# Kernel tuning notes

Measured on AMD Instinct MI355X. Metric: run time of the kernel, lower is better.

Reference implementation:

```python
import jax, jax.numpy as jnp
import numpy as np

B, S, D, H, E, K = 2, 2048, 512, 2048, 16, 2
LN_EPS = 1e-5


def setup_inputs() -> dict:
    key = jax.random.key(0)
    ks = jax.random.split(key, 9)
    s_in = 1.0 / np.sqrt(D)
    s_hid = 1.0 / np.sqrt(H)
    return {
        "x": jax.random.normal(ks[0], (B, S, D), dtype=jnp.float32),
        "Wg": jax.random.normal(ks[1], (D, E), dtype=jnp.float32) * s_in,
        "bg": jax.random.normal(ks[2], (E,), dtype=jnp.float32) * 0.01,
        "W1": jax.random.normal(ks[3], (E, D, H), dtype=jnp.float32) * s_in,
        "b1": jax.random.normal(ks[4], (E, H), dtype=jnp.float32) * 0.01,
        "W2": jax.random.normal(ks[5], (E, H, D), dtype=jnp.float32) * s_hid,
        "b2": jax.random.normal(ks[6], (E, D), dtype=jnp.float32) * 0.01,
        "gamma": jnp.ones((D,), dtype=jnp.float32),
        "beta": jnp.zeros((D,), dtype=jnp.float32),
    }


def reference(x, Wg, bg, W1, b1, W2, b2, gamma, beta):
    # --- top-k gating (GatingFuncTopK) ---
    logits = jnp.einsum("bsd,de->bse", x, Wg) + bg            # [B,S,E]
    probs = jax.nn.softmax(logits, axis=-1)
    topk_vals, topk_idx = jax.lax.top_k(probs, K)             # [B,S,K]
    # scatter top-k probs back into a sparse [B,S,E] routing matrix
    sparse = (jax.nn.one_hot(topk_idx, E, dtype=probs.dtype)
              * topk_vals[..., None]).sum(axis=-2)            # [B,S,E]

    # --- dense all-expert FFN (stack over experts, as in the torch code) ---
    h = jax.nn.relu(jnp.einsum("bsd,edh->ebsh", x, W1)
                    + b1[:, None, None, :])                   # [E,B,S,H]
    ex = jnp.einsum("ebsh,ehd->ebsd", h, W2) + b2[:, None, None, :]  # [E,B,S,D]

    # --- weighted combine + residual + layernorm ---
    out = jnp.einsum("bse,ebsd->bsd", sparse, ex) + x
    mu = out.mean(axis=-1, keepdims=True)
    var = ((out - mu) ** 2).mean(axis=-1, keepdims=True)
    out = (out - mu) * jax.lax.rsqrt(var + LN_EPS) * gamma + beta
    return out
```

## Files before the change

### kernel.cpp

```cpp
#include <hip/hip_runtime.h>
#include <math.h>

#define NTOK 4096
#define DDIM 512
#define HDIM 2048
#define NEXP 16


#define WS_COUNTS    0u
#define WS_OFFSETS   1024u
#define WS_NTILES    1280u
#define WS_TM        1536u
#define WS_EPOS      4096u
#define WS_TOK       36864u
#define WS_WL        299008u
#define WS_XA        1048576u
#define WS_W1T       11534336u
#define WS_W2T       45088768u
#define WS_HB        78643200u
#define WS_YB        WS_W1T

typedef __attribute__((ext_vector_type(8))) short short8;
typedef __attribute__((ext_vector_type(4))) float floatx4;
typedef unsigned short ushort_t;

__device__ __forceinline__ ushort_t f2bf(float f) {
    unsigned u = __float_as_uint(f);
    u += 0x7fffu + ((u >> 16) & 1u);
    return (ushort_t)(u >> 16);
}
__device__ __forceinline__ float bf2f(ushort_t u) {
    return __uint_as_float((unsigned)u << 16);
}

__device__ __forceinline__ void gld16(const void* g, void* l) {
    __builtin_amdgcn_global_load_lds(
        (const __attribute__((address_space(1))) unsigned*)g,
        (__attribute__((address_space(3))) unsigned*)l, 16, 0, 0);
}

#define WAIT4_BAR() asm volatile("s_waitcnt vmcnt(4)\n\ts_barrier" ::: "memory")
#define WAIT0_BAR() asm volatile("s_waitcnt vmcnt(0)\n\ts_barrier" ::: "memory")

__device__ __forceinline__ void wtrans_tile(
    const float* __restrict__ src, ushort_t* __restrict__ dst,
    int C, int NT, int CK, int e, int ks, int nw, unsigned* lb, int tid)
{
    const int q = tid >> 4;
    const int c0 = (tid & 15) << 2;
    const float* sp = src + (size_t)e * (DDIM * HDIM)
                    + (size_t)(ks * 32 + 2 * q) * C + nw * 256;
    float4 va[4], vb[4];
    #pragma unroll
    for (int p = 0; p < 4; ++p) {
        va[p] = *(const float4*)(sp + c0 + p * 64);
        vb[p] = *(const float4*)(sp + C + c0 + p * 64);
    }
    #pragma unroll
    for (int p = 0; p < 4; ++p) {
        const int n = c0 + p * 64;
        lb[(n + 0) * 17 + q] = (unsigned)f2bf(va[p].x) | ((unsigned)f2bf(vb[p].x) << 16);
        lb[(n + 1) * 17 + q] = (unsigned)f2bf(va[p].y) | ((unsigned)f2bf(vb[p].y) << 16);
        lb[(n + 2) * 17 + q] = (unsigned)f2bf(va[p].z) | ((unsigned)f2bf(vb[p].z) << 16);
        lb[(n + 3) * 17 + q] = (unsigned)f2bf(va[p].w) | ((unsigned)f2bf(vb[p].w) << 16);
    }
    __syncthreads();
    const int nt = tid >> 4, nl = tid & 15;
    const int ntg = nw * 16 + nt;
    ushort_t* rbase = dst + ((size_t)e * NT + ntg) * ((size_t)CK * 128) + nl * 8;
    const unsigned* rp = lb + (nt * 16 + nl) * 17;
    #pragma unroll
    for (int kc = 0; kc < 4; ++kc) {
        const unsigned o0 = rp[kc * 4 + 0], o1 = rp[kc * 4 + 1];
        const unsigned o2 = rp[kc * 4 + 2], o3 = rp[kc * 4 + 3];
        *(uint4*)(rbase + (size_t)(ks * 4 + kc) * 128) = make_uint4(o0, o1, o2, o3);
    }
}

__global__ __launch_bounds__(256) void fusedA_kernel(
    const float* __restrict__ x, const float* __restrict__ Wg,
    const float* __restrict__ bg, int* __restrict__ counts,
    int* __restrict__ tok_list, float* __restrict__ w_list,
    int* __restrict__ epos, const float* __restrict__ W1,
    ushort_t* __restrict__ W1t)
{
    __shared__ __align__(16) float smem[4416];
    __shared__ int lcnt[16], lbase[16];
    const int tid = threadIdx.x;
    int bid = blockIdx.x;

    if (bid >= 512) {
        bid -= 512;
        const int e = bid >> 7, r = bid & 127;
        const int nw = r & 7, ks = r >> 3;
        wtrans_tile(W1, W1t, HDIM, 128, 64, e, ks, nw, (unsigned*)smem, tid);
        return;
    }

    float (*xs)[520] = (float(*)[520])smem;
    float (*lsm)[16][2] = (float(*)[16][2])(smem + 4160);
    const int t0 = bid * 8;
    const float* xg = x + (size_t)t0 * DDIM;
    #pragma unroll
    for (int p = 0; p < 4; ++p) {
        const int idx = p * 1024 + tid * 4;
        *(float4*)&xs[idx >> 9][idx & 511] = *(const float4*)(xg + idx);
    }
    if (tid < 16) lcnt[tid] = 0;
    __syncthreads();
    const int tl = tid >> 5, e = (tid >> 1) & 15, h = tid & 1;
    float a0 = 0.f, a1 = 0.f, a2 = 0.f, a3 = 0.f;
    #pragma unroll 8
    for (int it = 0; it < 64; ++it) {
        const int d = h * 256 + it * 4;
        const float4 xv = *(const float4*)&xs[tl][d];
        a0 = fmaf(xv.x, Wg[(d + 0) * 16 + e], a0);
        a1 = fmaf(xv.y, Wg[(d + 1) * 16 + e], a1);
        a2 = fmaf(xv.z, Wg[(d + 2) * 16 + e], a2);
        a3 = fmaf(xv.w, Wg[(d + 3) * 16 + e], a3);
    }
    lsm[tl][e][h] = (a0 + a1) + (a2 + a3);
    __syncthreads();

    int i0 = 0, i1 = -1, r0 = 0, r1 = 0;
    float w0 = 0.f, w1 = 0.f;
    const bool tokth = ((tid & 31) == 0);
    if (tokth) {
        float l[16];
        #pragma unroll
        for (int j = 0; j < NEXP; ++j) l[j] = lsm[tl][j][0] + lsm[tl][j][1] + bg[j];
        float m = -1e30f;
        #pragma unroll
        for (int j = 0; j < NEXP; ++j) m = fmaxf(m, l[j]);
        float s = 0.f;
        #pragma unroll
        for (int j = 0; j < NEXP; ++j) s += __expf(l[j] - m);
        float v0 = -1e30f;
        #pragma unroll
        for (int j = 0; j < NEXP; ++j)
            if (l[j] > v0) { v0 = l[j]; i0 = j; }
        float v1 = -1e30f;
        #pragma unroll
        for (int j = 0; j < NEXP; ++j)
            if (j != i0 && l[j] > v1) { v1 = l[j]; i1 = j; }
        w0 = __expf(v0 - m) / s;
        w1 = __expf(v1 - m) / s;
        r0 = atomicAdd(&lcnt[i0], 1);
        r1 = atomicAdd(&lcnt[i1], 1);
    }
    __syncthreads();
    if (tid < 16 && lcnt[tid] > 0)
        lbase[tid] = atomicAdd(&counts[tid * 16], lcnt[tid]);
    __syncthreads();
    if (tokth) {
        const int t = t0 + tl;
        const int p0 = lbase[i0] + r0;
        tok_list[i0 * NTOK + p0] = t;
        w_list[i0 * NTOK + p0] = w0;
        epos[t * 2 + 0] = (i0 << 16) | p0;
        const int p1 = lbase[i1] + r1;
        tok_list[i1 * NTOK + p1] = t;
        w_list[i1 * NTOK + p1] = w1;
        epos[t * 2 + 1] = (i1 << 16) | p1;
    }
}

__global__ void scan_kernel(const int* __restrict__ counts, int* __restrict__ offsets,
                            int* __restrict__ tm, int* __restrict__ ntiles)
{
    const int lane = threadIdx.x;
    int c = (lane < NEXP) ? counts[lane * 16] : 0;
    int t = (c + 127) >> 7;
    int ic = c, it = t;
    #pragma unroll
    for (int off = 1; off < 16; off <<= 1) {
        const int pc = __shfl_up(ic, off, 64);
        const int pt = __shfl_up(it, off, 64);
        if (lane >= off) { ic += pc; it += pt; }
    }
    if (lane < NEXP) {
        offsets[lane] = ic - c;
        if (lane == NEXP - 1) { offsets[NEXP] = ic; ntiles[0] = it; }
        const int tb = it - t;
        for (int i = 0; i < t; ++i) tm[tb + i] = (lane << 16) | i;
    }
}

__global__ __launch_bounds__(256) void gather_xa(
    const float* __restrict__ x, const int* __restrict__ tok_list,
    const int* __restrict__ counts, const int* __restrict__ tm,
    const int* __restrict__ ntiles, ushort_t* __restrict__ xa)
{
    const int b = blockIdx.x;
    if (b >= ntiles[0]) return;
    const int info = tm[b];
    const int e = info >> 16, m0 = (info & 0xffff) << 7;
    const int Me = counts[e * 16];
    const int row = threadIdx.x >> 1;
    const int half = threadIdx.x & 1;
    const int kbase = blockIdx.y * 128 + half * 64;
    const int tok = tok_list[e * NTOK + min(m0 + row, Me - 1)];
    const float* src = x + (size_t)tok * DDIM + kbase;
    ushort_t* dstb = xa + (size_t)b * 65536 + (size_t)(row >> 4) * 8192 + (row & 15) * 8;
    #pragma unroll
    for (int q = 0; q < 16; ++q) {
        const int k = kbase + q * 4;
        const float4 v = *(const float4*)(src + q * 4);
        ushort4 o = make_ushort4(f2bf(v.x), f2bf(v.y), f2bf(v.z), f2bf(v.w));
        *(ushort4*)(dstb + (size_t)(k >> 3) * 128 + (k & 7)) = o;
    }
}

__global__ __launch_bounds__(256) void fusedC_kernel(
    const ushort_t* __restrict__ xa, const ushort_t* __restrict__ W1t,
    const float* __restrict__ b1, const int* __restrict__ tm,
    const int* __restrict__ ntiles, ushort_t* __restrict__ hb,
    const float* __restrict__ W2, ushort_t* __restrict__ W2t)
{
    __shared__ __align__(16) ushort_t lds[24576];
    const int tid = threadIdx.x;
    const int bid = blockIdx.x;

    if (bid >= 1280) {
        const int wb = bid - 1280;
        const int e = wb >> 7, r = wb & 127;
        const int nw = r & 1, ks = r >> 1;
        wtrans_tile(W2, W2t, DDIM, 32, 256, e, ks, nw, (unsigned*)lds, tid);
        return;
    }

    const int swz = (bid & 7) * 160 + (bid >> 3);
    const int t = swz >> 4;
    if (t >= ntiles[0]) return;
    const int e = tm[t] >> 16;
    const int n0 = (swz & 15) << 7;
    const int lane = tid & 63, w = tid >> 6;
    const int fm = lane & 15, fq = lane >> 4;
    const int wr = (w >> 1) << 6, wc = (w & 1) << 6;

    const ushort_t* gA = xa + (size_t)t * 65536 + lane * 8;
    const ushort_t* gB = W1t + ((size_t)e * 128 + (n0 >> 4)) * 8192 + lane * 8;
    const int s0 = w, s1 = w + 4;

    #define G1_STAGE(d, kc) do {                                            \
        ushort_t* lb_ = &lds[(d) * 8192];                                   \
        gld16(gA + (size_t)s0 * 8192 + (kc) * 512, lb_ + s0 * 512);         \
        gld16(gA + (size_t)s1 * 8192 + (kc) * 512, lb_ + s1 * 512);         \
        gld16(gB + (size_t)s0 * 8192 + (kc) * 512, lb_ + 4096 + s0 * 512);  \
        gld16(gB + (size_t)s1 * 8192 + (kc) * 512, lb_ + 4096 + s1 * 512);  \
    } while (0)

    #define G1_COMPUTE(cur) do {                                            \
        const ushort_t* la = &lds[(cur) * 8192 + ((w >> 1) * 4) * 512 + lane * 8]; \
        const ushort_t* lbB = &lds[(cur) * 8192 + 4096 + ((w & 1) * 4) * 512 + lane * 8]; \
        short8 af[4], bf[4];                                                \
        _Pragma("unroll")                                                   \
        for (int i = 0; i < 4; ++i) af[i] = *(const short8*)(la + i * 512); \
        _Pragma("unroll")                                                   \
        for (int j = 0; j < 4; ++j) bf[j] = *(const short8*)(lbB + j * 512);\
        _Pragma("unroll")                                                   \
        for (int i = 0; i < 4; ++i)                                         \
            _Pragma("unroll")                                               \
            for (int j = 0; j < 4; ++j)                                     \
                acc[i][j] = __builtin_amdgcn_mfma_f32_16x16x32_bf16(        \
                    af[i], bf[j], acc[i][j], 0, 0, 0);                      \
    } while (0)

    G1_STAGE(0, 0);
    G1_STAGE(1, 1);
    floatx4 acc[4][4] = {};
    int cur = 0;
    #pragma unroll 1
    for (int kc = 0; kc < 14; ++kc) {
        WAIT4_BAR();
        const int nb = (kc + 2) % 3;
        G1_STAGE(nb, kc + 2);
        G1_COMPUTE(cur);
        cur = (cur == 2) ? 0 : cur + 1;
    }
    WAIT4_BAR();
    G1_COMPUTE(cur);
    cur = (cur == 2) ? 0 : cur + 1;
    WAIT0_BAR();
    G1_COMPUTE(cur);
    __syncthreads();
    #undef G1_STAGE
    #undef G1_COMPUTE

    ushort_t* ls = lds;
    #pragma unroll
    for (int j = 0; j < 4; ++j) {
        const float bias = b1[(size_t)e * HDIM + n0 + wc + j * 16 + fm];
        #pragma unroll
        for (int i = 0; i < 4; ++i)
            #pragma unroll
            for (int r = 0; r < 4; ++r) {
                const int row = wr + i * 16 + fq * 4 + r;
                ls[row * 128 + wc + j * 16 + fm] =
                    f2bf(fmaxf(acc[i][j][r] + bias, 0.f));
            }
    }
    __syncthreads();
    ushort_t* hbase = hb + (size_t)t * 262144 + (size_t)(n0 >> 3) * 128;
    #pragma unroll
    for (int p = 0; p < 8; ++p) {
        const int unit = tid + p * 256;
        const int row = unit >> 4, c16 = unit & 15;
        *(short8*)(hbase + (size_t)(row >> 4) * 32768 + (size_t)c16 * 128
                   + (row & 15) * 8) = *(const short8*)&ls[row * 128 + c16 * 8];
    }
}

__global__ __launch_bounds__(256) void gemm2_mfma(
    const ushort_t* __restrict__ hb, const ushort_t* __restrict__ W2t,
    const float* __restrict__ b2, const float* __restrict__ w_list,
    const int* __restrict__ counts, const int* __restrict__ offsets,
    const int* __restrict__ tm, const int* __restrict__ ntiles,
    ushort_t* __restrict__ yb)
{
    const int bid = blockIdx.x;
    const int swz = (bid & 7) * 160 + (bid >> 3);
    const int n0i = swz & 3;
    const int q = swz >> 2;
    const int kz = q / 80;
    const int t = q - kz * 80;
    if (t >= ntiles[0]) return;
    const int info = tm[t];
    const int e = info >> 16, m0 = (info & 0xffff) << 7;
    const int Me = counts[e * 16], aoff = offsets[e];
    const int n0 = n0i << 7;
    const int tid = threadIdx.x, lane = tid & 63, w = tid >> 6;
    const int fm = lane & 15, fq = lane >> 4;
    const int wr = (w >> 1) << 6, wc = (w & 1) << 6;

    __shared__ __align__(16) ushort_t lds[24576];

    const ushort_t* gA = hb + (size_t)t * 262144 + (size_t)kz * 8192 + lane * 8;
    const ushort_t* gB = W2t + ((size_t)e * 32 + (n0 >> 4)) * 32768
                       + (size_t)kz * 8192 + lane * 8;
    const int s0 = w, s1 = w + 4;

    #define G2_STAGE(d, kc) do {                                            \
        ushort_t* lb_ = &lds[(d) * 8192];                                   \
        gld16(gA + (size_t)s0 * 32768 + (kc) * 512, lb_ + s0 * 512);        \
        gld16(gA + (size_t)s1 * 32768 + (kc) * 512, lb_ + s1 * 512);        \
        gld16(gB + (size_t)s0 * 32768 + (kc) * 512, lb_ + 4096 + s0 * 512); \
        gld16(gB + (size_t)s1 * 32768 + (kc) * 512, lb_ + 4096 + s1 * 512); \
    } while (0)

    #define G2_COMPUTE(cur) do {                                            \
        const ushort_t* la = &lds[(cur) * 8192 + ((w >> 1) * 4) * 512 + lane * 8]; \
        const ushort_t* lbB = &lds[(cur) * 8192 + 4096 + ((w & 1) * 4) * 512 + lane * 8]; \
        short8 af[4], bf[4];                                                \
        _Pragma("unroll")                                                   \
        for (int i = 0; i < 4; ++i) af[i] = *(const short8*)(la + i * 512); \
        _Pragma("unroll")                                                   \
        for (int j = 0; j < 4; ++j) bf[j] = *(const short8*)(lbB + j * 512);\
        _Pragma("unroll")                                                   \
        for (int i = 0; i < 4; ++i)                                         \
            _Pragma("unroll")                                               \
            for (int j = 0; j < 4; ++j)                                     \
                acc[i][j] = __builtin_amdgcn_mfma_f32_16x16x32_bf16(        \
                    af[i], bf[j], acc[i][j], 0, 0, 0);                      \
    } while (0)

    G2_STAGE(0, 0);
    G2_STAGE(1, 1);
    floatx4 acc[4][4] = {};
    int cur = 0;
    #pragma unroll 1
    for (int kc = 0; kc < 14; ++kc) {
        WAIT4_BAR();
        const int nb = (kc + 2) % 3;
        G2_STAGE(nb, kc + 2);
        G2_COMPUTE(cur);
        cur = (cur == 2) ? 0 : cur + 1;
    }
    WAIT4_BAR();
    G2_COMPUTE(cur);
    cur = (cur == 2) ? 0 : cur + 1;
    WAIT0_BAR();
    G2_COMPUTE(cur);
    __syncthreads();
    #undef G2_STAGE
    #undef G2_COMPUTE

    ushort_t* ls = lds;
    #pragma unroll
    for (int j = 0; j < 4; ++j) {
        const float bias = (kz == 0) ? b2[(size_t)e * DDIM + n0 + wc + j * 16 + fm] : 0.f;
        #pragma unroll
        for (int i = 0; i < 4; ++i)
            #pragma unroll
            for (int r = 0; r < 4; ++r) {
                const int row = wr + i * 16 + fq * 4 + r;
                const float gw = w_list[e * NTOK + min(m0 + row, Me - 1)];
                ls[row * 128 + wc + j * 16 + fm] = f2bf(gw * (acc[i][j][r] + bias));
            }
    }
    __syncthreads();
    ushort_t* ybase = yb + (size_t)kz * (8192 * 512) + n0;
    #pragma unroll
    for (int p = 0; p < 8; ++p) {
        const int unit = tid + p * 256;
        const int row = unit >> 4, c16 = unit & 15;
        if (m0 + row < Me)
            *(short8*)(ybase + (size_t)(aoff + m0 + row) * 512 + c16 * 8)
                = *(const short8*)&ls[row * 128 + c16 * 8];
    }
}

__global__ __launch_bounds__(256) void ln_kernel(
    const float* __restrict__ x, const ushort_t* __restrict__ yb,
    const int* __restrict__ epos, const int* __restrict__ offsets,
    const float* __restrict__ gamma, const float* __restrict__ beta,
    float* __restrict__ out)
{
    const int t = blockIdx.x * 4 + (threadIdx.x >> 6);
    const int lane = threadIdx.x & 63;
    const int d0 = lane * 8;

    const int p0 = epos[2 * t + 0];
    const int p1 = epos[2 * t + 1];
    const size_t r0 = (size_t)(offsets[p0 >> 16] + (p0 & 0xFFFF));
    const size_t r1 = (size_t)(offsets[p1 >> 16] + (p1 & 0xFFFF));

    short8 ys[8];
    #pragma unroll
    for (int kz = 0; kz < 4; ++kz) {
        ys[kz * 2 + 0] = *(const short8*)(yb + (size_t)kz * (8192 * 512) + r0 * 512 + d0);
        ys[kz * 2 + 1] = *(const short8*)(yb + (size_t)kz * (8192 * 512) + r1 * 512 + d0);
    }
    float xv[8];
    *(float4*)&xv[0] = *(const float4*)(x + (size_t)t * DDIM + d0);
    *(float4*)&xv[4] = *(const float4*)(x + (size_t)t * DDIM + d0 + 4);

    float v[8];
    float s = 0.f;
    #pragma unroll
    for (int i = 0; i < 8; ++i) {
        float a = xv[i];
        #pragma unroll
        for (int q = 0; q < 8; ++q) a += bf2f((ushort_t)ys[q][i]);
        v[i] = a;
        s += a;
    }
    #pragma unroll
    for (int o = 32; o > 0; o >>= 1) s += __shfl_xor(s, o, 64);
    const float mu = s * (1.f / DDIM);
    float q = 0.f;
    #pragma unroll
    for (int i = 0; i < 8; ++i) { const float d_ = v[i] - mu; q = fmaf(d_, d_, q); }
    #pragma unroll
    for (int o = 32; o > 0; o >>= 1) q += __shfl_xor(q, o, 64);
    const float rstd = rsqrtf(q * (1.f / DDIM) + 1e-5f);

    float g[8], bt[8], o8[8];
    *(float4*)&g[0] = *(const float4*)(gamma + d0);
    *(float4*)&g[4] = *(const float4*)(gamma + d0 + 4);
    *(float4*)&bt[0] = *(const float4*)(beta + d0);
    *(float4*)&bt[4] = *(const float4*)(beta + d0 + 4);
    #pragma unroll
    for (int i = 0; i < 8; ++i) o8[i] = (v[i] - mu) * rstd * g[i] + bt[i];
    *(float4*)(out + (size_t)t * DDIM + d0) = *(float4*)&o8[0];
    *(float4*)(out + (size_t)t * DDIM + d0 + 4) = *(float4*)&o8[4];
}

extern "C" void kernel_launch(void* const* d_in, const int* in_sizes, int n_in,
                              void* d_out, int out_size, void* d_ws, size_t ws_size,
                              hipStream_t stream) {
    const float* x     = (const float*)d_in[0];
    const float* Wg    = (const float*)d_in[1];
    const float* bg    = (const float*)d_in[2];
    const float* W1    = (const float*)d_in[3];
    const float* b1    = (const float*)d_in[4];
    const float* W2    = (const float*)d_in[5];
    const float* b2    = (const float*)d_in[6];
    const float* gamma = (const float*)d_in[7];
    const float* beta  = (const float*)d_in[8];
    float* out = (float*)d_out;

    char* ws = (char*)d_ws;
    int*      counts   = (int*)(ws + WS_COUNTS);
    int*      offsets  = (int*)(ws + WS_OFFSETS);
    int*      ntiles   = (int*)(ws + WS_NTILES);
    int*      tm       = (int*)(ws + WS_TM);
    int*      epos     = (int*)(ws + WS_EPOS);
    int*      tok_list = (int*)(ws + WS_TOK);
    float*    w_list   = (float*)(ws + WS_WL);
    ushort_t* xa       = (ushort_t*)(ws + WS_XA);
    ushort_t* W1t      = (ushort_t*)(ws + WS_W1T);
    ushort_t* W2t      = (ushort_t*)(ws + WS_W2T);
    ushort_t* hb       = (ushort_t*)(ws + WS_HB);
    ushort_t* yb       = (ushort_t*)(ws + WS_YB);

    hipMemsetAsync(counts, 0, 1024, stream);
    fusedA_kernel<<<2560, 256, 0, stream>>>(x, Wg, bg, counts, tok_list, w_list,
                                            epos, W1, W1t);
    scan_kernel<<<1, 64, 0, stream>>>(counts, offsets, tm, ntiles);
    gather_xa<<<dim3(80, 4), 256, 0, stream>>>(x, tok_list, counts, tm, ntiles, xa);
    fusedC_kernel<<<3328, 256, 0, stream>>>(xa, W1t, b1, tm, ntiles, hb, W2, W2t);
    gemm2_mfma<<<1280, 256, 0, stream>>>(
        hb, W2t, b2, w_list, counts, offsets, tm, ntiles, yb);
    ln_kernel<<<NTOK / 4, 256, 0, stream>>>(x, yb, epos, offsets, gamma, beta, out);
}
```

Baseline: 263.2 us.

## Fuse fp32 weight bf16 conversion into grouped GEMM B-tile loads

Removes the separate passes that transposed and converted W1 and W2 to bf16 into workspace, which were folded into the gating and GEMM1 launches. Each GEMM now reads fp32 weight rows directly into registers, packs them to bf16 and writes them transposed into a double-buffered padded LDS tile, while activations still stream through a triple-buffered async-to-LDS pipeline. This saves the extra write and read of the bf16 weight copies. In exchange, each GEMM tile reads fp32 weights, twice the bytes, and does the conversion per tile, so weights shared by many token tiles are converted repeatedly. Launch bounds requesting 3 blocks per CU were also added.

Measured after the change: 279.1 us. +6.0%, slower.

```diff
diff --git a/kernel.cpp b/kernel.cpp
--- a/kernel.cpp
+++ b/kernel.cpp
@@ -15,10 +15,8 @@
 #define WS_TOK       36864u
 #define WS_WL        299008u
 #define WS_XA        1048576u
-#define WS_W1T       11534336u
-#define WS_W2T       45088768u
+#define WS_YB        11534336u
 #define WS_HB        78643200u
-#define WS_YB        WS_W1T
 
 typedef __attribute__((ext_vector_type(8))) short short8;
 typedef __attribute__((ext_vector_type(4))) float floatx4;
@@ -32,6 +30,9 @@
 __device__ __forceinline__ float bf2f(ushort_t u) {
     return __uint_as_float((unsigned)u << 16);
 }
+__device__ __forceinline__ unsigned pk2(float a, float b) {
+    return (unsigned)f2bf(a) | ((unsigned)f2bf(b) << 16);
+}
 
 __device__ __forceinline__ void gld16(const void* g, void* l) {
     __builtin_amdgcn_global_load_lds(
@@ -39,63 +40,22 @@
         (__attribute__((address_space(3))) unsigned*)l, 16, 0, 0);
 }
 
-#define WAIT4_BAR() asm volatile("s_waitcnt vmcnt(4)\n\ts_barrier" ::: "memory")
-#define WAIT0_BAR() asm volatile("s_waitcnt vmcnt(0)\n\ts_barrier" ::: "memory")
-
-__device__ __forceinline__ void wtrans_tile(
-    const float* __restrict__ src, ushort_t* __restrict__ dst,
-    int C, int NT, int CK, int e, int ks, int nw, unsigned* lb, int tid)
-{
-    const int q = tid >> 4;
-    const int c0 = (tid & 15) << 2;
-    const float* sp = src + (size_t)e * (DDIM * HDIM)
-                    + (size_t)(ks * 32 + 2 * q) * C + nw * 256;
-    float4 va[4], vb[4];
-    #pragma unroll
-    for (int p = 0; p < 4; ++p) {
-        va[p] = *(const float4*)(sp + c0 + p * 64);
-        vb[p] = *(const float4*)(sp + C + c0 + p * 64);
-    }
-    #pragma unroll
-    for (int p = 0; p < 4; ++p) {
-        const int n = c0 + p * 64;
-        lb[(n + 0) * 17 + q] = (unsigned)f2bf(va[p].x) | ((unsigned)f2bf(vb[p].x) << 16);
-        lb[(n + 1) * 17 + q] = (unsigned)f2bf(va[p].y) | ((unsigned)f2bf(vb[p].y) << 16);
-        lb[(n + 2) * 17 + q] = (unsigned)f2bf(va[p].z) | ((unsigned)f2bf(vb[p].z) << 16);
-        lb[(n + 3) * 17 + q] = (unsigned)f2bf(va[p].w) | ((unsigned)f2bf(vb[p].w) << 16);
-    }
-    __syncthreads();
-    const int nt = tid >> 4, nl = tid & 15;
-    const int ntg = nw * 16 + nt;
-    ushort_t* rbase = dst + ((size_t)e * NT + ntg) * ((size_t)CK * 128) + nl * 8;
-    const unsigned* rp = lb + (nt * 16 + nl) * 17;
-    #pragma unroll
-    for (int kc = 0; kc < 4; ++kc) {
-        const unsigned o0 = rp[kc * 4 + 0], o1 = rp[kc * 4 + 1];
-        const unsigned o2 = rp[kc * 4 + 2], o3 = rp[kc * 4 + 3];
-        *(uint4*)(rbase + (size_t)(ks * 4 + kc) * 128) = make_uint4(o0, o1, o2, o3);
-    }
-}
-
-__global__ __launch_bounds__(256) void fusedA_kernel(
+#define WAIT2()  asm volatile("s_waitcnt vmcnt(2)" ::: "memory")
+#define WAIT0()  asm volatile("s_waitcnt vmcnt(0)" ::: "memory")
+#define LGKM_BAR() asm volatile("s_waitcnt lgkmcnt(0)\n\ts_barrier" ::: "memory")
+
+union U8 { unsigned u[4]; short8 s; };
+
+__global__ __launch_bounds__(256) void gating_kernel(
     const float* __restrict__ x, const float* __restrict__ Wg,
     const float* __restrict__ bg, int* __restrict__ counts,
     int* __restrict__ tok_list, float* __restrict__ w_list,
-    int* __restrict__ epos, const float* __restrict__ W1,
-    ushort_t* __restrict__ W1t)
+    int* __restrict__ epos)
 {
     __shared__ __align__(16) float smem[4416];
     __shared__ int lcnt[16], lbase[16];
     const int tid = threadIdx.x;
-    int bid = blockIdx.x;
-
-    if (bid >= 512) {
-        bid -= 512;
-        const int e = bid >> 7, r = bid & 127;
-        const int nw = r & 7, ks = r >> 3;
-        wtrans_tile(W1, W1t, HDIM, 128, 64, e, ks, nw, (unsigned*)smem, tid);
-        return;
-    }
+    const int bid = blockIdx.x;
 
     float (*xs)[520] = (float(*)[520])smem;
     float (*lsm)[16][2] = (float(*)[16][2])(smem + 4160);
@@ -211,81 +171,106 @@
     }
 }
 
-__global__ __launch_bounds__(256) void fusedC_kernel(
-    const ushort_t* __restrict__ xa, const ushort_t* __restrict__ W1t,
+__global__ __launch_bounds__(256, 3) void gemm1_mfma(
+    const ushort_t* __restrict__ xa, const float* __restrict__ W1,
     const float* __restrict__ b1, const int* __restrict__ tm,
-    const int* __restrict__ ntiles, ushort_t* __restrict__ hb,
-    const float* __restrict__ W2, ushort_t* __restrict__ W2t)
+    const int* __restrict__ ntiles, ushort_t* __restrict__ hb)
 {
-    __shared__ __align__(16) ushort_t lds[24576];
-    const int tid = threadIdx.x;
     const int bid = blockIdx.x;
-
-    if (bid >= 1280) {
-        const int wb = bid - 1280;
-        const int e = wb >> 7, r = wb & 127;
-        const int nw = r & 1, ks = r >> 1;
-        wtrans_tile(W2, W2t, DDIM, 32, 256, e, ks, nw, (unsigned*)lds, tid);
-        return;
-    }
-
     const int swz = (bid & 7) * 160 + (bid >> 3);
     const int t = swz >> 4;
     if (t >= ntiles[0]) return;
     const int e = tm[t] >> 16;
     const int n0 = (swz & 15) << 7;
-    const int lane = tid & 63, w = tid >> 6;
+    const int tid = threadIdx.x, lane = tid & 63, w = tid >> 6;
     const int fm = lane & 15, fq = lane >> 4;
     const int wr = (w >> 1) << 6, wc = (w & 1) << 6;
 
+    __shared__ __align__(16) ushort_t lds[20992];
+    ushort_t* Al = lds;
+    unsigned* Bb = (unsigned*)(lds + 12288);
+
     const ushort_t* gA = xa + (size_t)t * 65536 + lane * 8;
-    const ushort_t* gB = W1t + ((size_t)e * 128 + (n0 >> 4)) * 8192 + lane * 8;
     const int s0 = w, s1 = w + 4;
-
-    #define G1_STAGE(d, kc) do {                                            \
-        ushort_t* lb_ = &lds[(d) * 8192];                                   \
-        gld16(gA + (size_t)s0 * 8192 + (kc) * 512, lb_ + s0 * 512);         \
-        gld16(gA + (size_t)s1 * 8192 + (kc) * 512, lb_ + s1 * 512);         \
-        gld16(gB + (size_t)s0 * 8192 + (kc) * 512, lb_ + 4096 + s0 * 512);  \
-        gld16(gB + (size_t)s1 * 8192 + (kc) * 512, lb_ + 4096 + s1 * 512);  \
-    } while (0)
-
-    #define G1_COMPUTE(cur) do {                                            \
-        const ushort_t* la = &lds[(cur) * 8192 + ((w >> 1) * 4) * 512 + lane * 8]; \
-        const ushort_t* lbB = &lds[(cur) * 8192 + 4096 + ((w & 1) * 4) * 512 + lane * 8]; \
-        short8 af[4], bf[4];                                                \
+    const float* gB = W1 + (size_t)e * (DDIM * HDIM) + n0;
+    const int qa = tid >> 5, ca4 = (tid & 31) << 2;
+
+    float4 bvv[4];
+
+    #define AGLD(k) do {                                                    \
+        ushort_t* ab_ = Al + ((k) % 3) * 4096;                              \
+        gld16(gA + (size_t)s0 * 8192 + (k) * 512, ab_ + s0 * 512);          \
+        gld16(gA + (size_t)s1 * 8192 + (k) * 512, ab_ + s1 * 512);          \
+    } while (0)
+
+    #define BLOAD(k) do {                                                   \
+        const float* r0_ = gB + (size_t)((k) * 32 + 2 * qa) * HDIM + ca4;   \
+        const float* r1_ = gB + (size_t)((k) * 32 + 2 * qa + 16) * HDIM + ca4; \
+        bvv[0] = *(const float4*)r0_;                                       \
+        bvv[1] = *(const float4*)(r0_ + HDIM);                              \
+        bvv[2] = *(const float4*)r1_;                                       \
+        bvv[3] = *(const float4*)(r1_ + HDIM);                              \
+    } while (0)
+
+    #define BWRITE(k) do {                                                  \
+        unsigned* BL_ = Bb + ((k) & 1) * 2176;                              \
+        BL_[(ca4 + 0) * 17 + qa] = pk2(bvv[0].x, bvv[1].x);                 \
+        BL_[(ca4 + 1) * 17 + qa] = pk2(bvv[0].y, bvv[1].y);                 \
+        BL_[(ca4 + 2) * 17 + qa] = pk2(bvv[0].z, bvv[1].z);                 \
+        BL_[(ca4 + 3) * 17 + qa] = pk2(bvv[0].w, bvv[1].w);                 \
+        BL_[(ca4 + 0) * 17 + qa + 8] = pk2(bvv[2].x, bvv[3].x);             \
+        BL_[(ca4 + 1) * 17 + qa + 8] = pk2(bvv[2].y, bvv[3].y);             \
+        BL_[(ca4 + 2) * 17 + qa + 8] = pk2(bvv[2].z, bvv[3].z);             \
+        BL_[(ca4 + 3) * 17 + qa + 8] = pk2(bvv[2].w, bvv[3].w);             \
+    } while (0)
+
+    #define COMPUTE(k) do {                                                 \
+        const ushort_t* la_ = Al + ((k) % 3) * 4096 + ((w >> 1) * 4) * 512 + lane * 8; \
+        const unsigned* bb_ = Bb + ((k) & 1) * 2176                         \
+                            + ((w & 1) * 64 + (lane & 15)) * 17 + (lane >> 4) * 4; \
+        short8 af[4];                                                       \
         _Pragma("unroll")                                                   \
-        for (int i = 0; i < 4; ++i) af[i] = *(const short8*)(la + i * 512); \
+        for (int i = 0; i < 4; ++i) af[i] = *(const short8*)(la_ + i * 512);\
         _Pragma("unroll")                                                   \
-        for (int j = 0; j < 4; ++j) bf[j] = *(const short8*)(lbB + j * 512);\
-        _Pragma("unroll")                                                   \
-        for (int i = 0; i < 4; ++i)                                         \
+        for (int j = 0; j < 4; ++j) {                                       \
+            U8 tb_;                                                         \
+            tb_.u[0] = bb_[j * 272 + 0]; tb_.u[1] = bb_[j * 272 + 1];       \
+            tb_.u[2] = bb_[j * 272 + 2]; tb_.u[3] = bb_[j * 272 + 3];       \
+            const short8 bf_ = tb_.s;                                       \
             _Pragma("unroll")                                               \
-            for (int j = 0; j < 4; ++j)                                     \
+            for (int i = 0; i < 4; ++i)                                     \
                 acc[i][j] = __builtin_amdgcn_mfma_f32_16x16x32_bf16(        \
-                    af[i], bf[j], acc[i][j], 0, 0, 0);                      \
-    } while (0)
-
-    G1_STAGE(0, 0);
-    G1_STAGE(1, 1);
+                    af[i], bf_, acc[i][j], 0, 0, 0);                        \
+        }                                                                   \
+    } while (0)
+
+    #define STEP(k, WM) do {                                                \
+        WM();                              \
+        BWRITE(k);                                                          \
+        LGKM_BAR();                                                         \
+        if ((k) < 15) BLOAD((k) + 1);                                       \
+        if ((k) < 14) AGLD((k) + 2);                                        \
+        COMPUTE(k);                                                         \
+    } while (0)
+
+    BLOAD(0);
+    AGLD(0);
+    AGLD(1);
+
     floatx4 acc[4][4] = {};
-    int cur = 0;
     #pragma unroll 1
-    for (int kc = 0; kc < 14; ++kc) {
-        WAIT4_BAR();
-        const int nb = (kc + 2) % 3;
-        G1_STAGE(nb, kc + 2);
-        G1_COMPUTE(cur);
-        cur = (cur == 2) ? 0 : cur + 1;
-    }
-    WAIT4_BAR();
-    G1_COMPUTE(cur);
-    cur = (cur == 2) ? 0 : cur + 1;
-    WAIT0_BAR();
-    G1_COMPUTE(cur);
-    __syncthreads();
-    #undef G1_STAGE
-    #undef G1_COMPUTE
+    for (int kc = 0; kc < 14; kc += 2) {
+        STEP(kc, WAIT2);
+        STEP(kc + 1, WAIT2);
+    }
+    STEP(14, WAIT2);
+    STEP(15, WAIT0);
+    __syncthreads();
+    #undef AGLD
+    #undef BLOAD
+    #undef BWRITE
+    #undef COMPUTE
+    #undef STEP
 
     ushort_t* ls = lds;
     #pragma unroll
@@ -311,8 +296,8 @@
     }
 }
 
-__global__ __launch_bounds__(256) void gemm2_mfma(
-    const ushort_t* __restrict__ hb, const ushort_t* __restrict__ W2t,
+__global__ __launch_bounds__(256, 3) void gemm2_mfma(
+    const ushort_t* __restrict__ hb, const float* __restrict__ W2,
     const float* __restrict__ b2, const float* __restrict__ w_list,
     const int* __restrict__ counts, const int* __restrict__ offsets,
     const int* __restrict__ tm, const int* __restrict__ ntiles,
@@ -321,9 +306,9 @@
     const int bid = blockIdx.x;
     const int swz = (bid & 7) * 160 + (bid >> 3);
     const int n0i = swz & 3;
-    const int q = swz >> 2;
-    const int kz = q / 80;
-    const int t = q - kz * 80;
+    const int q_ = swz >> 2;
+    const int kz = q_ / 80;
+    const int t = q_ - kz * 80;
     if (t >= ntiles[0]) return;
     const int info = tm[t];
     const int e = info >> 16, m0 = (info & 0xffff) << 7;
@@ -333,57 +318,91 @@
     const int fm = lane & 15, fq = lane >> 4;
     const int wr = (w >> 1) << 6, wc = (w & 1) << 6;
 
-    __shared__ __align__(16) ushort_t lds[24576];
+    __shared__ __align__(16) ushort_t lds[20992];
+    ushort_t* Al = lds;
+    unsigned* Bb = (unsigned*)(lds + 12288);
 
     const ushort_t* gA = hb + (size_t)t * 262144 + (size_t)kz * 8192 + lane * 8;
-    const ushort_t* gB = W2t + ((size_t)e * 32 + (n0 >> 4)) * 32768
-                       + (size_t)kz * 8192 + lane * 8;
     const int s0 = w, s1 = w + 4;
-
-    #define G2_STAGE(d, kc) do {                                            \
-        ushort_t* lb_ = &lds[(d) * 8192];                                   \
-        gld16(gA + (size_t)s0 * 32768 + (kc) * 512, lb_ + s0 * 512);        \
-        gld16(gA + (size_t)s1 * 32768 + (kc) * 512, lb_ + s1 * 512);        \
-        gld16(gB + (size_t)s0 * 32768 + (kc) * 512, lb_ + 4096 + s0 * 512); \
-        gld16(gB + (size_t)s1 * 32768 + (kc) * 512, lb_ + 4096 + s1 * 512); \
-    } while (0)
-
-    #define G2_COMPUTE(cur) do {                                            \
-        const ushort_t* la = &lds[(cur) * 8192 + ((w >> 1) * 4) * 512 + lane * 8]; \
-        const ushort_t* lbB = &lds[(cur) * 8192 + 4096 + ((w & 1) * 4) * 512 + lane * 8]; \
-        short8 af[4], bf[4];                                                \
+    const float* gB = W2 + (size_t)e * (DDIM * HDIM) + (size_t)kz * 512 * DDIM + n0;
+    const int qa = tid >> 5, ca4 = (tid & 31) << 2;
+
+    float4 bvv[4];
+
+    #define AGLD(k) do {                                                    \
+        ushort_t* ab_ = Al + ((k) % 3) * 4096;                              \
+        gld16(gA + (size_t)s0 * 32768 + (k) * 512, ab_ + s0 * 512);         \
+        gld16(gA + (size_t)s1 * 32768 + (k) * 512, ab_ + s1 * 512);         \
+    } while (0)
+
+    #define BLOAD(k) do {                                                   \
+        const float* r0_ = gB + (size_t)((k) * 32 + 2 * qa) * DDIM + ca4;   \
+        const float* r1_ = gB + (size_t)((k) * 32 + 2 * qa + 16) * DDIM + ca4; \
+        bvv[0] = *(const float4*)r0_;                                       \
+        bvv[1] = *(const float4*)(r0_ + DDIM);                              \
+        bvv[2] = *(const float4*)r1_;                                       \
+        bvv[3] = *(const float4*)(r1_ + DDIM);                              \
+    } while (0)
+
+    #define BWRITE(k) do {                                                  \
+        unsigned* BL_ = Bb + ((k) & 1) * 2176;                              \
+        BL_[(ca4 + 0) * 17 + qa] = pk2(bvv[0].x, bvv[1].x);                 \
+        BL_[(ca4 + 1) * 17 + qa] = pk2(bvv[0].y, bvv[1].y);                 \
+        BL_[(ca4 + 2) * 17 + qa] = pk2(bvv[0].z, bvv[1].z);                 \
+        BL_[(ca4 + 3) * 17 + qa] = pk2(bvv[0].w, bvv[1].w);                 \
+        BL_[(ca4 + 0) * 17 + qa + 8] = pk2(bvv[2].x, bvv[3].x);             \
+        BL_[(ca4 + 1) * 17 + qa + 8] = pk2(bvv[2].y, bvv[3].y);             \
+        BL_[(ca4 + 2) * 17 + qa + 8] = pk2(bvv[2].z, bvv[3].z);             \
+        BL_[(ca4 + 3) * 17 + qa + 8] = pk2(bvv[2].w, bvv[3].w);             \
+    } while (0)
+
+    #define COMPUTE(k) do {                                                 \
+        const ushort_t* la_ = Al + ((k) % 3) * 4096 + ((w >> 1) * 4) * 512 + lane * 8; \
+        const unsigned* bb_ = Bb + ((k) & 1) * 2176                         \
+                            + ((w & 1) * 64 + (lane & 15)) * 17 + (lane >> 4) * 4; \
+        short8 af[4];                                                       \
         _Pragma("unroll")                                                   \
-        for (int i = 0; i < 4; ++i) af[i] = *(const short8*)(la + i * 512); \
+        for (int i = 0; i < 4; ++i) af[i] = *(const short8*)(la_ + i * 512);\
         _Pragma("unroll")                                                   \
-        for (int j = 0; j < 4; ++j) bf[j] = *(const short8*)(lbB + j * 512);\
-        _Pragma("unroll")                                                   \
-        for (int i = 0; i < 4; ++i)                                         \
+        for (int j = 0; j < 4; ++j) {                                       \
+            U8 tb_;                                                         \
+            tb_.u[0] = bb_[j * 272 + 0]; tb_.u[1] = bb_[j * 272 + 1];       \
+            tb_.u[2] = bb_[j * 272 + 2]; tb_.u[3] = bb_[j * 272 + 3];       \
+            const short8 bf_ = tb_.s;                                       \
             _Pragma("unroll")                                               \
-            for (int j = 0; j < 4; ++j)                                     \
+            for (int i = 0; i < 4; ++i)                                     \
                 acc[i][j] = __builtin_amdgcn_mfma_f32_16x16x32_bf16(        \
-                    af[i], bf[j], acc[i][j], 0, 0, 0);                      \
-    } while (0)
-
-    G2_STAGE(0, 0);
-    G2_STAGE(1, 1);
+                    af[i], bf_, acc[i][j], 0, 0, 0);                        \
+        }                                                                   \
+    } while (0)
+
+    #define STEP(k, WM) do {                                                \
+        WM();                                                               \
+        BWRITE(k);                                                          \
+        LGKM_BAR();                                                         \
+        if ((k) < 15) BLOAD((k) + 1);                                       \
+        if ((k) < 14) AGLD((k) + 2);                                        \
+        COMPUTE(k);                                                         \
+    } while (0)
+
+    BLOAD(0);
+    AGLD(0);
+    AGLD(1);
+
     floatx4 acc[4][4] = {};
-    int cur = 0;
     #pragma unroll 1
-    for (int kc = 0; kc < 14; ++kc) {
-        WAIT4_BAR();
-        const int nb = (kc + 2) % 3;
-        G2_STAGE(nb, kc + 2);
-        G2_COMPUTE(cur);
-        cur = (cur == 2) ? 0 : cur + 1;
-    }
-    WAIT4_BAR();
-    G2_COMPUTE(cur);
-    cur = (cur == 2) ? 0 : cur + 1;
-    WAIT0_BAR();
-    G2_COMPUTE(cur);
-    __syncthreads();
-    #undef G2_STAGE
-    #undef G2_COMPUTE
+    for (int kc = 0; kc < 14; kc += 2) {
+        STEP(kc, WAIT2);
+        STEP(kc + 1, WAIT2);
+    }
+    STEP(14, WAIT2);
+    STEP(15, WAIT0);
+    __syncthreads();
+    #undef AGLD
+    #undef BLOAD
+    #undef BWRITE
+    #undef COMPUTE
+    #undef STEP
 
     ushort_t* ls = lds;
     #pragma unroll
@@ -489,18 +508,15 @@
     int*      tok_list = (int*)(ws + WS_TOK);
     float*    w_list   = (float*)(ws + WS_WL);
     ushort_t* xa       = (ushort_t*)(ws + WS_XA);
-    ushort_t* W1t      = (ushort_t*)(ws + WS_W1T);
-    ushort_t* W2t      = (ushort_t*)(ws + WS_W2T);
+    ushort_t* yb       = (ushort_t*)(ws + WS_YB);
     ushort_t* hb       = (ushort_t*)(ws + WS_HB);
-    ushort_t* yb       = (ushort_t*)(ws + WS_YB);
 
     hipMemsetAsync(counts, 0, 1024, stream);
-    fusedA_kernel<<<2560, 256, 0, stream>>>(x, Wg, bg, counts, tok_list, w_list,
-                                            epos, W1, W1t);
+    gating_kernel<<<512, 256, 0, stream>>>(x, Wg, bg, counts, tok_list, w_list, epos);
     scan_kernel<<<1, 64, 0, stream>>>(counts, offsets, tm, ntiles);
     gather_xa<<<dim3(80, 4), 256, 0, stream>>>(x, tok_list, counts, tm, ntiles, xa);
-    fusedC_kernel<<<3328, 256, 0, stream>>>(xa, W1t, b1, tm, ntiles, hb, W2, W2t);
-    gemm2_mfma<<<1280, 256, 0, stream>>>(
-        hb, W2t, b2, w_list, counts, offsets, tm, ntiles, yb);
+    gemm1_mfma<<<1280, 256, 0, stream>>>(xa, W1, b1, tm, ntiles, hb);
+    gemm2_mfma<<<1280, 256, 0, stream>>>(hb, W2, b2, w_list, counts, offsets,
+                                         tm, ntiles, yb);
     ln_kernel<<<NTOK / 4, 256, 0, stream>>>(x, yb, epos, offsets, gamma, beta, out);
 }
```

## Fuse token gather into GEMM1 and move W2 transpose into first kernel

Applied to the files above, without the earlier changes.

Removes the separate gather_xa kernel. GEMM1 now loads routed token rows of x directly from global memory, converts them to bf16 in registers and writes them into double-buffered LDS, while W1t tiles are still streamed asynchronously into a triple buffer. The W2 transpose work moves from the GEMM1 launch into the gating/W1-transpose kernel, so GEMM1 runs only GEMM tiles. Launch bounds are added for occupancy. The aim is to avoid the xa round trip through global memory and one kernel launch. The cost is register-based A loads that may stall the pipeline, plus a longer first kernel.

After: 299.8 us. 1.14x slower.

```diff
diff --git a/kernel.cpp b/kernel.cpp
--- a/kernel.cpp
+++ b/kernel.cpp
@@ -14,7 +14,6 @@
 #define WS_EPOS      4096u
 #define WS_TOK       36864u
 #define WS_WL        299008u
-#define WS_XA        1048576u
 #define WS_W1T       11534336u
 #define WS_W2T       45088768u
 #define WS_HB        78643200u
@@ -32,6 +31,9 @@
 __device__ __forceinline__ float bf2f(ushort_t u) {
     return __uint_as_float((unsigned)u << 16);
 }
+__device__ __forceinline__ unsigned pk2(float a, float b) {
+    return (unsigned)f2bf(a) | ((unsigned)f2bf(b) << 16);
+}
 
 __device__ __forceinline__ void gld16(const void* g, void* l) {
     __builtin_amdgcn_global_load_lds(
@@ -39,8 +41,10 @@
         (__attribute__((address_space(3))) unsigned*)l, 16, 0, 0);
 }
 
+#define WAIT6_BAR() asm volatile("s_waitcnt vmcnt(6)\n\ts_barrier" ::: "memory")
 #define WAIT4_BAR() asm volatile("s_waitcnt vmcnt(4)\n\ts_barrier" ::: "memory")
 #define WAIT0_BAR() asm volatile("s_waitcnt vmcnt(0)\n\ts_barrier" ::: "memory")
+#define LGKM_BAR()  asm volatile("s_waitcnt lgkmcnt(0)\n\ts_barrier" ::: "memory")
 
 __device__ __forceinline__ void wtrans_tile(
     const float* __restrict__ src, ushort_t* __restrict__ dst,
@@ -59,10 +63,10 @@
     #pragma unroll
     for (int p = 0; p < 4; ++p) {
         const int n = c0 + p * 64;
-        lb[(n + 0) * 17 + q] = (unsigned)f2bf(va[p].x) | ((unsigned)f2bf(vb[p].x) << 16);
-        lb[(n + 1) * 17 + q] = (unsigned)f2bf(va[p].y) | ((unsigned)f2bf(vb[p].y) << 16);
-        lb[(n + 2) * 17 + q] = (unsigned)f2bf(va[p].z) | ((unsigned)f2bf(vb[p].z) << 16);
-        lb[(n + 3) * 17 + q] = (unsigned)f2bf(va[p].w) | ((unsigned)f2bf(vb[p].w) << 16);
+        lb[(n + 0) * 17 + q] = pk2(va[p].x, vb[p].x);
+        lb[(n + 1) * 17 + q] = pk2(va[p].y, vb[p].y);
+        lb[(n + 2) * 17 + q] = pk2(va[p].z, vb[p].z);
+        lb[(n + 3) * 17 + q] = pk2(va[p].w, vb[p].w);
     }
     __syncthreads();
     const int nt = tid >> 4, nl = tid & 15;
@@ -82,13 +86,21 @@
     const float* __restrict__ bg, int* __restrict__ counts,
     int* __restrict__ tok_list, float* __restrict__ w_list,
     int* __restrict__ epos, const float* __restrict__ W1,
-    ushort_t* __restrict__ W1t)
+    ushort_t* __restrict__ W1t, const float* __restrict__ W2,
+    ushort_t* __restrict__ W2t)
 {
     __shared__ __align__(16) float smem[4416];
     __shared__ int lcnt[16], lbase[16];
     const int tid = threadIdx.x;
     int bid = blockIdx.x;
 
+    if (bid >= 2560) {
+        const int wb = bid - 2560;
+        const int e = wb >> 7, r = wb & 127;
+        const int nw = r & 1, ks = r >> 1;
+        wtrans_tile(W2, W2t, DDIM, 32, 256, e, ks, nw, (unsigned*)smem, tid);
+        return;
+    }
     if (bid >= 512) {
         bid -= 512;
         const int e = bid >> 7, r = bid & 127;
@@ -186,78 +198,70 @@
     }
 }
 
-__global__ __launch_bounds__(256) void gather_xa(
+__global__ __launch_bounds__(256, 4) void gemm1_mfma(
     const float* __restrict__ x, const int* __restrict__ tok_list,
+    const ushort_t* __restrict__ W1t, const float* __restrict__ b1,
     const int* __restrict__ counts, const int* __restrict__ tm,
-    const int* __restrict__ ntiles, ushort_t* __restrict__ xa)
+    const int* __restrict__ ntiles, ushort_t* __restrict__ hb)
 {
-    const int b = blockIdx.x;
-    if (b >= ntiles[0]) return;
-    const int info = tm[b];
-    const int e = info >> 16, m0 = (info & 0xffff) << 7;
-    const int Me = counts[e * 16];
-    const int row = threadIdx.x >> 1;
-    const int half = threadIdx.x & 1;
-    const int kbase = blockIdx.y * 128 + half * 64;
-    const int tok = tok_list[e * NTOK + min(m0 + row, Me - 1)];
-    const float* src = x + (size_t)tok * DDIM + kbase;
-    ushort_t* dstb = xa + (size_t)b * 65536 + (size_t)(row >> 4) * 8192 + (row & 15) * 8;
-    #pragma unroll
-    for (int q = 0; q < 16; ++q) {
-        const int k = kbase + q * 4;
-        const float4 v = *(const float4*)(src + q * 4);
-        ushort4 o = make_ushort4(f2bf(v.x), f2bf(v.y), f2bf(v.z), f2bf(v.w));
-        *(ushort4*)(dstb + (size_t)(k >> 3) * 128 + (k & 7)) = o;
-    }
-}
-
-__global__ __launch_bounds__(256) void fusedC_kernel(
-    const ushort_t* __restrict__ xa, const ushort_t* __restrict__ W1t,
-    const float* __restrict__ b1, const int* __restrict__ tm,
-    const int* __restrict__ ntiles, ushort_t* __restrict__ hb,
-    const float* __restrict__ W2, ushort_t* __restrict__ W2t)
-{
-    __shared__ __align__(16) ushort_t lds[24576];
-    const int tid = threadIdx.x;
     const int bid = blockIdx.x;
-
-    if (bid >= 1280) {
-        const int wb = bid - 1280;
-        const int e = wb >> 7, r = wb & 127;
-        const int nw = r & 1, ks = r >> 1;
-        wtrans_tile(W2, W2t, DDIM, 32, 256, e, ks, nw, (unsigned*)lds, tid);
-        return;
-    }
-
     const int swz = (bid & 7) * 160 + (bid >> 3);
     const int t = swz >> 4;
     if (t >= ntiles[0]) return;
-    const int e = tm[t] >> 16;
+    const int info = tm[t];
+    const int e = info >> 16, m0 = (info & 0xffff) << 7;
+    const int Me = counts[e * 16];
     const int n0 = (swz & 15) << 7;
-    const int lane = tid & 63, w = tid >> 6;
+    const int tid = threadIdx.x, lane = tid & 63, w = tid >> 6;
     const int fm = lane & 15, fq = lane >> 4;
     const int wr = (w >> 1) << 6, wc = (w & 1) << 6;
 
-    const ushort_t* gA = xa + (size_t)t * 65536 + lane * 8;
+    __shared__ __align__(16) ushort_t lds[20480];
+    ushort_t* Ab = lds;
+    ushort_t* Bb = lds + 8192;
+
+    const int r_ = tid >> 1, half = tid & 1;
+    const int tok = tok_list[e * NTOK + min(m0 + r_, Me - 1)];
+    const float* xrow = x + (size_t)tok * DDIM + half * 16;
+    const int awoff = (r_ >> 4) * 512 + half * 256 + (r_ & 15) * 8;
+
     const ushort_t* gB = W1t + ((size_t)e * 128 + (n0 >> 4)) * 8192 + lane * 8;
     const int s0 = w, s1 = w + 4;
 
-    #define G1_STAGE(d, kc) do {                                            \
-        ushort_t* lb_ = &lds[(d) * 8192];                                   \
-        gld16(gA + (size_t)s0 * 8192 + (kc) * 512, lb_ + s0 * 512);         \
-        gld16(gA + (size_t)s1 * 8192 + (kc) * 512, lb_ + s1 * 512);         \
-        gld16(gB + (size_t)s0 * 8192 + (kc) * 512, lb_ + 4096 + s0 * 512);  \
-        gld16(gB + (size_t)s1 * 8192 + (kc) * 512, lb_ + 4096 + s1 * 512);  \
-    } while (0)
-
-    #define G1_COMPUTE(cur) do {                                            \
-        const ushort_t* la = &lds[(cur) * 8192 + ((w >> 1) * 4) * 512 + lane * 8]; \
-        const ushort_t* lbB = &lds[(cur) * 8192 + 4096 + ((w & 1) * 4) * 512 + lane * 8]; \
+    float4 vA[2][4];
+
+    #define ALOAD(k) do {                                                   \
+        const float* xp_ = xrow + (k) * 32;                                 \
+        float4* v_ = vA[(k) & 1];                                           \
+        v_[0] = *(const float4*)(xp_ + 0);                                  \
+        v_[1] = *(const float4*)(xp_ + 4);                                  \
+        v_[2] = *(const float4*)(xp_ + 8);                                  \
+        v_[3] = *(const float4*)(xp_ + 12);                                 \
+    } while (0)
+
+    #define AWRITE(k) do {                                                  \
+        ushort_t* d_ = Ab + ((k) & 1) * 4096 + awoff;                       \
+        const float4* v_ = vA[(k) & 1];                                     \
+        *(uint4*)(d_) = make_uint4(pk2(v_[0].x, v_[0].y), pk2(v_[0].z, v_[0].w), \
+                                   pk2(v_[1].x, v_[1].y), pk2(v_[1].z, v_[1].w)); \
+        *(uint4*)(d_ + 128) = make_uint4(pk2(v_[2].x, v_[2].y), pk2(v_[2].z, v_[2].w), \
+                                         pk2(v_[3].x, v_[3].y), pk2(v_[3].z, v_[3].w)); \
+    } while (0)
+
+    #define BGLD(k) do {                                                    \
+        ushort_t* bb_ = Bb + ((k) % 3) * 4096;                              \
+        gld16(gB + (size_t)s0 * 8192 + (k) * 512, bb_ + s0 * 512);          \
+        gld16(gB + (size_t)s1 * 8192 + (k) * 512, bb_ + s1 * 512);          \
+    } while (0)
+
+    #define COMPUTE(k) do {                                                 \
+        const ushort_t* la_ = Ab + ((k) & 1) * 4096 + ((w >> 1) * 4) * 512 + lane * 8; \
+        const ushort_t* lb_ = Bb + ((k) % 3) * 4096 + ((w & 1) * 4) * 512 + lane * 8; \
         short8 af[4], bf[4];                                                \
         _Pragma("unroll")                                                   \
-        for (int i = 0; i < 4; ++i) af[i] = *(const short8*)(la + i * 512); \
+        for (int i = 0; i < 4; ++i) af[i] = *(const short8*)(la_ + i * 512);\
         _Pragma("unroll")                                                   \
-        for (int j = 0; j < 4; ++j) bf[j] = *(const short8*)(lbB + j * 512);\
+        for (int j = 0; j < 4; ++j) bf[j] = *(const short8*)(lb_ + j * 512);\
         _Pragma("unroll")                                                   \
         for (int i = 0; i < 4; ++i)                                         \
             _Pragma("unroll")                                               \
@@ -266,26 +270,31 @@
                     af[i], bf[j], acc[i][j], 0, 0, 0);                      \
     } while (0)
 
-    G1_STAGE(0, 0);
-    G1_STAGE(1, 1);
+    #define STEP(k, WM) do {                                                \
+        WM();                                                               \
+        AWRITE(k);                                                          \
+        LGKM_BAR();                                                         \
+        if ((k) < 14) { ALOAD((k) + 2); BGLD((k) + 2); }                    \
+        COMPUTE(k);                                                         \
+    } while (0)
+
+    ALOAD(0); BGLD(0);
+    ALOAD(1); BGLD(1);
+
     floatx4 acc[4][4] = {};
-    int cur = 0;
     #pragma unroll 1
-    for (int kc = 0; kc < 14; ++kc) {
-        WAIT4_BAR();
-        const int nb = (kc + 2) % 3;
-        G1_STAGE(nb, kc + 2);
-        G1_COMPUTE(cur);
-        cur = (cur == 2) ? 0 : cur + 1;
-    }
-    WAIT4_BAR();
-    G1_COMPUTE(cur);
-    cur = (cur == 2) ? 0 : cur + 1;
-    WAIT0_BAR();
-    G1_COMPUTE(cur);
-    __syncthreads();
-    #undef G1_STAGE
-    #undef G1_COMPUTE
+    for (int kc = 0; kc < 14; kc += 2) {
+        STEP(kc, WAIT6_BAR);
+        STEP(kc + 1, WAIT6_BAR);
+    }
+    STEP(14, WAIT6_BAR);
+    STEP(15, WAIT0_BAR);
+    __syncthreads();
+    #undef ALOAD
+    #undef AWRITE
+    #undef BGLD
+    #undef COMPUTE
+    #undef STEP
 
     ushort_t* ls = lds;
     #pragma unroll
@@ -311,7 +320,7 @@
     }
 }
 
-__global__ __launch_bounds__(256) void gemm2_mfma(
+__global__ __launch_bounds__(256, 3) void gemm2_mfma(
     const ushort_t* __restrict__ hb, const ushort_t* __restrict__ W2t,
     const float* __restrict__ b2, const float* __restrict__ w_list,
     const int* __restrict__ counts, const int* __restrict__ offsets,
@@ -321,9 +330,9 @@
     const int bid = blockIdx.x;
     const int swz = (bid & 7) * 160 + (bid >> 3);
     const int n0i = swz & 3;
-    const int q = swz >> 2;
-    const int kz = q / 80;
-    const int t = q - kz * 80;
+    const int q_ = swz >> 2;
+    const int kz = q_ / 80;
+    const int t = q_ - kz * 80;
     if (t >= ntiles[0]) return;
     const int info = tm[t];
     const int e = info >> 16, m0 = (info & 0xffff) << 7;
@@ -488,19 +497,18 @@
     int*      epos     = (int*)(ws + WS_EPOS);
     int*      tok_list = (int*)(ws + WS_TOK);
     float*    w_list   = (float*)(ws + WS_WL);
-    ushort_t* xa       = (ushort_t*)(ws + WS_XA);
     ushort_t* W1t      = (ushort_t*)(ws + WS_W1T);
     ushort_t* W2t      = (ushort_t*)(ws + WS_W2T);
     ushort_t* hb       = (ushort_t*)(ws + WS_HB);
     ushort_t* yb       = (ushort_t*)(ws + WS_YB);
 
     hipMemsetAsync(counts, 0, 1024, stream);
-    fusedA_kernel<<<2560, 256, 0, stream>>>(x, Wg, bg, counts, tok_list, w_list,
-                                            epos, W1, W1t);
+    fusedA_kernel<<<4608, 256, 0, stream>>>(x, Wg, bg, counts, tok_list, w_list,
+                                            epos, W1, W1t, W2, W2t);
     scan_kernel<<<1, 64, 0, stream>>>(counts, offsets, tm, ntiles);
-    gather_xa<<<dim3(80, 4), 256, 0, stream>>>(x, tok_list, counts, tm, ntiles, xa);
-    fusedC_kernel<<<3328, 256, 0, stream>>>(xa, W1t, b1, tm, ntiles, hb, W2, W2t);
-    gemm2_mfma<<<1280, 256, 0, stream>>>(
-        hb, W2t, b2, w_list, counts, offsets, tm, ntiles, yb);
+    gemm1_mfma<<<1280, 256, 0, stream>>>(x, tok_list, W1t, b1, counts, tm,
+                                         ntiles, hb);
+    gemm2_mfma<<<1280, 256, 0, stream>>>(hb, W2t, b2, w_list, counts, offsets,
+                                         tm, ntiles, yb);
     ln_kernel<<<NTOK / 4, 256, 0, stream>>>(x, yb, epos, offsets, gamma, beta, out);
 }
```
